# Optimization experiments

Hardware: AMD Instinct MI355X
Metric: run time of the kernel (lower is better)

## Reference

```python
import jax, jax.numpy as jnp
import numpy as np

EMB_DIM = 300
TEMPERATURE = 0.01
REWEIGHT = True
N = 8192
NUM_GROUPS = 100


def setup_inputs() -> dict:
    key = jax.random.key(0)
    ks = jax.random.split(key, 6)
    s = 1.0 / np.sqrt(EMB_DIM)
    x = jax.random.normal(ks[0], (N, EMB_DIM), dtype=jnp.float32)
    W1 = jax.random.normal(ks[1], (EMB_DIM, EMB_DIM), dtype=jnp.float32) * s
    b1 = jnp.zeros((EMB_DIM,), dtype=jnp.float32)
    W2 = jax.random.normal(ks[2], (EMB_DIM, EMB_DIM), dtype=jnp.float32) * s
    b2 = jnp.zeros((EMB_DIM,), dtype=jnp.float32)
    # labels in [1, 100]: all > 0 so the group_y>0 filter keeps every row
    labels = jax.random.randint(ks[3], (N,), 1, NUM_GROUPS + 1, dtype=jnp.int32)
    return {"x": x, "W1": W1, "b1": b1, "W2": W2, "b2": b2, "labels": labels}


def reference(x, W1, b1, W2, b2, labels):
    # projector: Linear -> ReLU -> Linear
    h = jax.nn.relu(x @ W1 + b1) @ W2 + b2
    # L2 normalize rows
    f = h / jnp.linalg.norm(h, axis=1, keepdims=True)
    # pairwise similarity / temperature, row-max subtracted (detached)
    logits = (f @ f.T) / TEMPERATURE                      # [N, N]
    logits = logits - jax.lax.stop_gradient(jnp.max(logits, axis=1, keepdims=True))

    lab = labels[:, None]
    mask = (lab == lab.T).astype(logits.dtype)            # same-group mask
    logits_mask = 1.0 - jnp.eye(mask.shape[0], dtype=logits.dtype)  # drop diagonal
    mask = mask * logits_mask

    # rows with at least one positive (torch filters these; we weight instead)
    pos_count = jnp.sum(mask, axis=1)                     # [N]
    valid = pos_count > 0

    if REWEIGHT:
        pos_m = logits_mask * mask
        neg_m = logits_mask * (1.0 - mask)
        pos_sum = jnp.sum(pos_m, axis=1, keepdims=True)
        neg_sum = jnp.sum(neg_m, axis=1, keepdims=True)
        log_pos = jnp.where(pos_sum > 0, jnp.log(jnp.maximum(pos_sum, 1.0)), 0.0)
        log_neg = jnp.where(neg_sum > 0, jnp.log(jnp.maximum(neg_sum, 1.0)), 0.0)
        logits = (logits - log_pos) * pos_m + (logits - log_neg) * neg_m

    exp_logits = jnp.exp(logits) * logits_mask
    log_prob = logits - jnp.log(jnp.sum(exp_logits, axis=1, keepdims=True))
    mean_log_prob_pos = jnp.sum(mask * log_prob, axis=1) / jnp.where(valid, pos_count, 1.0)
    validf = valid.astype(logits.dtype)
    loss = -TEMPERATURE * jnp.sum(mean_log_prob_pos * validf) / jnp.sum(validf)
    return loss
```

## Files before the change

kernel.cpp:

```cpp
#include <hip/hip_runtime.h>
#include <hip/hip_bf16.h>


#define N_ROWS 8192
#define D_PAD 320
#define NG 100
#define TEMP 0.01f
#define NSPLIT 32
#define JCHUNK (N_ROWS / NSPLIT)
#define LOG2E100 144.2695041f

typedef short short8v __attribute__((ext_vector_type(8)));
typedef float float4v __attribute__((ext_vector_type(4)));

__device__ __forceinline__ short f2bf(float f) {
  union { __hip_bfloat16 h; short s; } u;
  u.h = __float2bfloat16(f);
  return u.s;
}

__global__ __launch_bounds__(256) void setup_kernel(
    const float* __restrict__ W1, const float* __restrict__ W2,
    const int* __restrict__ labels,
    __hip_bfloat16* __restrict__ w1t, __hip_bfloat16* __restrict__ w2t,
    int* __restrict__ counts)
{
  __shared__ int hc[NG + 1];
  int b = blockIdx.x, tid = threadIdx.x;
  if (b < 800) {
    int isW2 = (b >= 400);
    int idx = (b - (isW2 ? 400 : 0)) * 256 + tid;
    const float* W = isW2 ? W2 : W1;
    __hip_bfloat16* dst = isW2 ? w2t : w1t;
    int n = idx / D_PAD, k = idx - n * D_PAD;
    float v = (n < 300 && k < 300) ? W[(size_t)k * 300 + n] : 0.0f;
    dst[idx] = __float2bfloat16(v);
  } else {
    if (tid <= NG) hc[tid] = 0;
    __syncthreads();
    int row = (b - 800) * 256 + tid;
    atomicAdd(&hc[labels[row]], 1);
    __syncthreads();
    if (tid <= NG && hc[tid] > 0) atomicAdd(&counts[tid], hc[tid]);
  }
}

__global__ __launch_bounds__(256, 2) void mlp_fused_kernel(
    const float* __restrict__ x, const __hip_bfloat16* __restrict__ w1t,
    const __hip_bfloat16* __restrict__ w2t, const float* __restrict__ b1,
    const float* __restrict__ b2, __hip_bfloat16* __restrict__ fb)
{
  __shared__ __align__(16) short Ws[64 * D_PAD];
  __shared__ __align__(16) short H1[64 * D_PAD];
  int tid = threadIdx.x;
  int lane = tid & 63, wave = tid >> 6;
  int g = lane >> 4, lc = lane & 15, sw = lc & 7;
  int i0 = blockIdx.x * 64;

  short8v afr[10];
  {
    const float* xp = x + (size_t)(i0 + wave * 16 + lc) * 300;
#pragma unroll
    for (int kk = 0; kk < 10; ++kk) {
      int k0 = kk * 32 + g * 8;
      short8v v;
      if (k0 + 8 <= 300) {
        float4 a = *(const float4*)(xp + k0);
        float4 c = *(const float4*)(xp + k0 + 4);
        v[0] = f2bf(a.x); v[1] = f2bf(a.y); v[2] = f2bf(a.z); v[3] = f2bf(a.w);
        v[4] = f2bf(c.x); v[5] = f2bf(c.y); v[6] = f2bf(c.z); v[7] = f2bf(c.w);
      } else if (k0 < 300) {
        float4 a = *(const float4*)(xp + k0);
        v[0] = f2bf(a.x); v[1] = f2bf(a.y); v[2] = f2bf(a.z); v[3] = f2bf(a.w);
        v[4] = 0; v[5] = 0; v[6] = 0; v[7] = 0;
      } else {
        v = short8v{0, 0, 0, 0, 0, 0, 0, 0};
      }
      afr[kk] = v;
    }
  }

  for (int c = 0; c < 5; ++c) {
    __syncthreads();
    {
      const int4* src = (const int4*)w1t;
      int4* dst = (int4*)Ws;
#pragma unroll
      for (int t = 0; t < 10; ++t) {
        int e = tid + t * 256;
        int r = e / 40, q = e - r * 40;
        dst[r * 40 + (q ^ (r & 7))] = src[(size_t)(c * 64 + r) * 40 + q];
      }
    }
    __syncthreads();
    for (int js = 0; js < 4; ++js) {
      float4v acc = {0.f, 0.f, 0.f, 0.f};
      const short* rowp = Ws + (js * 16 + lc) * D_PAD;
#pragma unroll
      for (int kk = 0; kk < 10; ++kk) {
        short8v bf = *(const short8v*)(rowp + (((g + 4 * kk) ^ sw) << 3));
        acc = __builtin_amdgcn_mfma_f32_16x16x32_bf16(afr[kk], bf, acc, 0, 0, 0);
      }
      int n = c * 64 + js * 16 + lc;
      float bv = (n < 300) ? b1[n] : 0.0f;
#pragma unroll
      for (int r = 0; r < 4; ++r) {
        int row = wave * 16 + g * 4 + r;
        int q = n >> 3;
        H1[row * D_PAD + ((q ^ (row & 7)) << 3) + (n & 7)] =
            f2bf(fmaxf(acc[r] + bv, 0.0f));
      }
    }
  }
  __syncthreads();

  short8v hfr[10];
  {
    const short* rp = H1 + (wave * 16 + lc) * D_PAD;
#pragma unroll
    for (int kk = 0; kk < 10; ++kk)
      hfr[kk] = *(const short8v*)(rp + (((g + 4 * kk) ^ sw) << 3));
  }

  float4v h2a[5][4];
  for (int c = 0; c < 5; ++c) {
    __syncthreads();
    {
      const int4* src = (const int4*)w2t;
      int4* dst = (int4*)Ws;
#pragma unroll
      for (int t = 0; t < 10; ++t) {
        int e = tid + t * 256;
        int r = e / 40, q = e - r * 40;
        dst[r * 40 + (q ^ (r & 7))] = src[(size_t)(c * 64 + r) * 40 + q];
      }
    }
    __syncthreads();
#pragma unroll
    for (int js = 0; js < 4; ++js) {
      float4v acc = {0.f, 0.f, 0.f, 0.f};
      const short* rowp = Ws + (js * 16 + lc) * D_PAD;
#pragma unroll
      for (int kk = 0; kk < 10; ++kk) {
        short8v bf = *(const short8v*)(rowp + (((g + 4 * kk) ^ sw) << 3));
        acc = __builtin_amdgcn_mfma_f32_16x16x32_bf16(hfr[kk], bf, acc, 0, 0, 0);
      }
      int n = c * 64 + js * 16 + lc;
      float bv = (n < 300) ? b2[n] : 0.0f;
#pragma unroll
      for (int r = 0; r < 4; ++r) acc[r] += bv;
      h2a[c][js] = acc;
    }
  }

  float ssq[4] = {0.f, 0.f, 0.f, 0.f};
#pragma unroll
  for (int c = 0; c < 5; ++c)
#pragma unroll
    for (int js = 0; js < 4; ++js)
#pragma unroll
      for (int r = 0; r < 4; ++r) ssq[r] = fmaf(h2a[c][js][r], h2a[c][js][r], ssq[r]);
  for (int m = 1; m < 16; m <<= 1)
#pragma unroll
    for (int r = 0; r < 4; ++r) ssq[r] += __shfl_xor(ssq[r], m, 64);
  float inv[4];
#pragma unroll
  for (int r = 0; r < 4; ++r) inv[r] = rsqrtf(ssq[r]);
#pragma unroll
  for (int c = 0; c < 5; ++c)
#pragma unroll
    for (int js = 0; js < 4; ++js) {
      int n = c * 64 + js * 16 + lc;
#pragma unroll
      for (int r = 0; r < 4; ++r) {
        int row = i0 + wave * 16 + g * 4 + r;
        fb[(size_t)row * D_PAD + n] = __float2bfloat16(h2a[c][js][r] * inv[r]);
      }
    }
}

__global__ __launch_bounds__(256) void group_kernel(
    const __hip_bfloat16* __restrict__ Fb, const int* __restrict__ labels,
    float* __restrict__ sPar, float* __restrict__ sAar)
{
  __shared__ __align__(16) short Bs[64 * D_PAD];
  __shared__ int memb[256];
  __shared__ int cnt;
  const short* Fs = (const short*)Fb;
  int tid = threadIdx.x;
  int lane = tid & 63, wave = tid >> 6;
  int g = lane >> 4, lc = lane & 15, sw = lc & 7;
  int grp = blockIdx.x + 1;
  if (tid == 0) cnt = 0;
  __syncthreads();
  for (int i = tid; i < N_ROWS; i += 256)
    if (labels[i] == grp) { int p = atomicAdd(&cnt, 1); if (p < 256) memb[p] = i; }
  __syncthreads();
  int c = cnt > 256 ? 256 : cnt;
  int nt = (c + 63) >> 6;
  for (int it = 0; it < nt; ++it) {
    short8v afr[10];
    {
      int islot = it * 64 + wave * 16 + lc;
      int arow = memb[islot < c ? islot : 0];
      const short* ap = Fs + (size_t)arow * D_PAD + g * 8;
#pragma unroll
      for (int kk = 0; kk < 10; ++kk) afr[kk] = *(const short8v*)(ap + kk * 32);
    }
    int iglobr[4]; bool ivalid[4];
    for (int r = 0; r < 4; ++r) {
      int islot = it * 64 + wave * 16 + g * 4 + r;
      ivalid[r] = islot < c;
      iglobr[r] = memb[islot < c ? islot : 0];
    }
    float sp[4] = {}, sa[4] = {};
    for (int jt = 0; jt < nt; ++jt) {
      __syncthreads();
      {
        const int4* src = (const int4*)Fs;
        int4* dst = (int4*)Bs;
#pragma unroll
        for (int t = 0; t < 10; ++t) {
          int e = tid + t * 256;
          int r = e / 40, q = e - r * 40;
          int jslot = jt * 64 + r;
          int grow = memb[jslot < c ? jslot : 0];
          dst[r * 40 + (q ^ (r & 7))] = src[(size_t)grow * 40 + q];
        }
      }
      __syncthreads();
      for (int js = 0; js < 4; ++js) {
        float4v acc = {0.f, 0.f, 0.f, 0.f};
        const short* rowp = Bs + (js * 16 + lc) * D_PAD;
#pragma unroll
        for (int kk = 0; kk < 10; ++kk) {
          short8v bf = *(const short8v*)(rowp + (((g + 4 * kk) ^ sw) << 3));
          acc = __builtin_amdgcn_mfma_f32_16x16x32_bf16(afr[kk], bf, acc, 0, 0, 0);
        }
        int jslot = jt * 64 + js * 16 + lc;
        bool jv = jslot < c;
        int jglob = memb[jslot < c ? jslot : 0];
#pragma unroll
        for (int r = 0; r < 4; ++r) {
          float a = acc[r];
          float e = exp2f(fmaf(a, LOG2E100, -LOG2E100));
          bool ok = jv && ivalid[r] && (jglob != iglobr[r]);
          sp[r] += ok ? e : 0.f;
          sa[r] += ok ? a : 0.f;
        }
      }
    }
    for (int m = 1; m < 16; m <<= 1)
      for (int r = 0; r < 4; ++r) {
        sp[r] += __shfl_xor(sp[r], m, 64);
        sa[r] += __shfl_xor(sa[r], m, 64);
      }
    if (lc == 0)
      for (int r = 0; r < 4; ++r)
        if (ivalid[r]) { sPar[iglobr[r]] = sp[r]; sAar[iglobr[r]] = sa[r]; }
  }
}

__global__ __launch_bounds__(256, 2) void pairwise_kernel(
    const __hip_bfloat16* __restrict__ Fb, float* __restrict__ partE)
{
  __shared__ __align__(16) short Bs[64 * D_PAD];
  const short* Fs = (const short*)Fb;
  int tid = threadIdx.x;
  int lane = tid & 63, wave = tid >> 6;
  int g = lane >> 4, lc = lane & 15, sw = lc & 7;
  int i0 = blockIdx.x * 128;
  int split = blockIdx.y;
  int jstart = split * JCHUNK;

  short8v afr[2][10];
  for (int s = 0; s < 2; ++s) {
    const short* ap = Fs + (size_t)(i0 + s * 64 + wave * 16 + lc) * D_PAD + g * 8;
#pragma unroll
    for (int kk = 0; kk < 10; ++kk) afr[s][kk] = *(const short8v*)(ap + kk * 32);
  }
  float sE[2][4] = {};

  for (int jt = 0; jt < JCHUNK / 64; ++jt) {
    int jb = jstart + jt * 64;
    __syncthreads();
    {
      const int4* src = (const int4*)Fs;
      int4* dst = (int4*)Bs;
#pragma unroll
      for (int t = 0; t < 10; ++t) {
        int e = tid + t * 256;
        int r = e / 40, q = e - r * 40;
        dst[r * 40 + (q ^ (r & 7))] = src[(size_t)(jb + r) * 40 + q];
      }
    }
    __syncthreads();
    for (int js = 0; js < 4; ++js) {
      float4v acc0 = {0.f, 0.f, 0.f, 0.f}, acc1 = {0.f, 0.f, 0.f, 0.f};
      const short* rowp = Bs + (js * 16 + lc) * D_PAD;
#pragma unroll
      for (int kk = 0; kk < 10; ++kk) {
        short8v bf = *(const short8v*)(rowp + (((g + 4 * kk) ^ sw) << 3));
        acc0 = __builtin_amdgcn_mfma_f32_16x16x32_bf16(afr[0][kk], bf, acc0, 0, 0, 0);
        acc1 = __builtin_amdgcn_mfma_f32_16x16x32_bf16(afr[1][kk], bf, acc1, 0, 0, 0);
      }
#pragma unroll
      for (int s = 0; s < 2; ++s) {
        float4v acc = s ? acc1 : acc0;
        bool dtile = (jb == i0 + s * 64) && (js == wave);
#pragma unroll
        for (int r = 0; r < 4; ++r) {
          float e = exp2f(fmaf(acc[r], LOG2E100, -LOG2E100));
          if (dtile && lc == g * 4 + r) e = 0.0f;
          sE[s][r] += e;
        }
      }
    }
  }
  for (int m = 1; m < 16; m <<= 1)
    for (int s = 0; s < 2; ++s)
      for (int r = 0; r < 4; ++r) sE[s][r] += __shfl_xor(sE[s][r], m, 64);
  if (lc == 0)
    for (int s = 0; s < 2; ++s)
      for (int r = 0; r < 4; ++r)
        partE[split * N_ROWS + i0 + s * 64 + wave * 16 + g * 4 + r] = sE[s][r];
}

__global__ __launch_bounds__(256) void final_a_kernel(
    const float* __restrict__ partE, const float* __restrict__ sPar,
    const float* __restrict__ sAar, const int* __restrict__ counts,
    const int* __restrict__ labels, float* __restrict__ blk)
{
  int tid = threadIdx.x;
  int i = blockIdx.x * 256 + tid;
  float sE = 0.f;
  for (int s = 0; s < NSPLIT; ++s) sE += partE[s * N_ROWS + i];
  float M = 0.f, V = 0.f;
  int pc = counts[labels[i]] - 1;
  if (pc > 0) {
    float P = sPar[i], A = sAar[i];
    float Q = sE - P;
    float pcf = (float)pc, ncf = (float)(N_ROWS - 1 - pc);
    float Z = P / pcf + Q / ncf;
    M = 100.0f * A / pcf - 100.0f - logf(pcf) - logf(Z);
    V = 1.f;
  }
  __shared__ float rm[256], rv[256];
  rm[tid] = M; rv[tid] = V;
  __syncthreads();
  for (int s2 = 128; s2 > 0; s2 >>= 1) {
    if (tid < s2) { rm[tid] += rm[tid + s2]; rv[tid] += rv[tid + s2]; }
    __syncthreads();
  }
  if (tid == 0) { blk[blockIdx.x] = rm[0]; blk[32 + blockIdx.x] = rv[0]; }
}

__global__ void final_b_kernel(const float* __restrict__ blk, float* __restrict__ out)
{
  int lane = threadIdx.x;
  float m = (lane < 32) ? blk[lane] : 0.f;
  float v = (lane < 32) ? blk[32 + lane] : 0.f;
  for (int s = 1; s < 32; s <<= 1) { m += __shfl_xor(m, s, 64); v += __shfl_xor(v, s, 64); }
  if (lane == 0) out[0] = (v > 0.f) ? (-TEMP * m / v) : 0.f;
}

extern "C" void kernel_launch(void* const* d_in, const int* in_sizes, int n_in,
                              void* d_out, int out_size, void* d_ws, size_t ws_size,
                              hipStream_t stream)
{
  const float* x  = (const float*)d_in[0];
  const float* W1 = (const float*)d_in[1];
  const float* b1 = (const float*)d_in[2];
  const float* W2 = (const float*)d_in[3];
  const float* b2 = (const float*)d_in[4];
  const int* labels = (const int*)d_in[5];

  char* ws = (char*)d_ws;
  __hip_bfloat16* fb  = (__hip_bfloat16*)(ws);
  __hip_bfloat16* w1t = (__hip_bfloat16*)(ws + 5242880);
  __hip_bfloat16* w2t = (__hip_bfloat16*)(ws + 5447680);
  int*         counts = (int*)(ws + 5652480);
  float*        partE = (float*)(ws + 5652992);
  float*        sPar  = (float*)(ws + 6701568);
  float*        sAar  = (float*)(ws + 6734336);
  float*        blk   = (float*)(ws + 6767104);

  hipMemsetAsync(counts, 0, (NG + 1) * sizeof(int), stream);
  setup_kernel<<<832, 256, 0, stream>>>(W1, W2, labels, w1t, w2t, counts);
  mlp_fused_kernel<<<N_ROWS / 64, 256, 0, stream>>>(x, w1t, w2t, b1, b2, fb);
  group_kernel<<<NG, 256, 0, stream>>>(fb, labels, sPar, sAar);
  pairwise_kernel<<<dim3(N_ROWS / 128, NSPLIT), 256, 0, stream>>>(fb, partE);
  final_a_kernel<<<32, 256, 0, stream>>>(partE, sPar, sAar, counts, labels, blk);
  final_b_kernel<<<1, 64, 0, stream>>>(blk, (float*)d_out);
}
```

Measured before the change: 174.8 us.

## Exploit Gram symmetry, fuse group and pairwise kernels, merge final reductions

The pairwise exp-sum kernel now computes only upper-triangular 128x128 tiles and adds each tile's column sums into the mirrored rows with atomics, roughly halving the MFMA and exp work. The group kernel runs inside the same launch as extra blocks so both overlap. The weight transpose uses an LDS tile for coalesced access, the MLP kernel uses 32-row blocks with 128 threads for more blocks, and the two final reduction kernels become one. Atomics on row sums add contention, and early-returning blocks waste part of the grid.

Measured after the change: 233.5 us. +33.6%, slower.

```diff
diff --git a/kernel.cpp b/kernel.cpp
--- a/kernel.cpp
+++ b/kernel.cpp
@@ -6,8 +6,6 @@
 #define D_PAD 320
 #define NG 100
 #define TEMP 0.01f
-#define NSPLIT 32
-#define JCHUNK (N_ROWS / NSPLIT)
 #define LOG2E100 144.2695041f
 
 typedef short short8v __attribute__((ext_vector_type(8)));
@@ -25,37 +23,50 @@
     __hip_bfloat16* __restrict__ w1t, __hip_bfloat16* __restrict__ w2t,
     int* __restrict__ counts)
 {
+  __shared__ float T[64][65];
   __shared__ int hc[NG + 1];
   int b = blockIdx.x, tid = threadIdx.x;
-  if (b < 800) {
-    int isW2 = (b >= 400);
-    int idx = (b - (isW2 ? 400 : 0)) * 256 + tid;
+  if (b < 50) {
+    int isW2 = b >= 25;
+    int t5 = isW2 ? b - 25 : b;
+    int k0 = (t5 / 5) * 64, n0 = (t5 % 5) * 64;
     const float* W = isW2 ? W2 : W1;
     __hip_bfloat16* dst = isW2 ? w2t : w1t;
-    int n = idx / D_PAD, k = idx - n * D_PAD;
-    float v = (n < 300 && k < 300) ? W[(size_t)k * 300 + n] : 0.0f;
-    dst[idx] = __float2bfloat16(v);
+#pragma unroll
+    for (int t = 0; t < 16; ++t) {
+      int e = tid + t * 256;
+      int r = e >> 6, c = e & 63;
+      T[r][c] = (k0 + r < 300 && n0 + c < 300)
+                  ? W[(size_t)(k0 + r) * 300 + (n0 + c)] : 0.0f;
+    }
+    __syncthreads();
+#pragma unroll
+    for (int t = 0; t < 16; ++t) {
+      int e = tid + t * 256;
+      int nn = e >> 6, kk = e & 63;
+      dst[(size_t)(n0 + nn) * D_PAD + (k0 + kk)] = __float2bfloat16(T[kk][nn]);
+    }
   } else {
     if (tid <= NG) hc[tid] = 0;
     __syncthreads();
-    int row = (b - 800) * 256 + tid;
+    int row = (b - 50) * 256 + tid;
     atomicAdd(&hc[labels[row]], 1);
     __syncthreads();
     if (tid <= NG && hc[tid] > 0) atomicAdd(&counts[tid], hc[tid]);
   }
 }
 
-__global__ __launch_bounds__(256, 2) void mlp_fused_kernel(
+__global__ __launch_bounds__(128, 2) void mlp_fused_kernel(
     const float* __restrict__ x, const __hip_bfloat16* __restrict__ w1t,
     const __hip_bfloat16* __restrict__ w2t, const float* __restrict__ b1,
     const float* __restrict__ b2, __hip_bfloat16* __restrict__ fb)
 {
   __shared__ __align__(16) short Ws[64 * D_PAD];
-  __shared__ __align__(16) short H1[64 * D_PAD];
+  __shared__ __align__(16) short H1[32 * D_PAD];
   int tid = threadIdx.x;
   int lane = tid & 63, wave = tid >> 6;
   int g = lane >> 4, lc = lane & 15, sw = lc & 7;
-  int i0 = blockIdx.x * 64;
+  int i0 = blockIdx.x * 32;
 
   short8v afr[10];
   {
@@ -86,8 +97,8 @@
       const int4* src = (const int4*)w1t;
       int4* dst = (int4*)Ws;
 #pragma unroll
-      for (int t = 0; t < 10; ++t) {
-        int e = tid + t * 256;
+      for (int t = 0; t < 20; ++t) {
+        int e = tid + t * 128;
         int r = e / 40, q = e - r * 40;
         dst[r * 40 + (q ^ (r & 7))] = src[(size_t)(c * 64 + r) * 40 + q];
       }
@@ -129,8 +140,8 @@
       const int4* src = (const int4*)w2t;
       int4* dst = (int4*)Ws;
 #pragma unroll
-      for (int t = 0; t < 10; ++t) {
-        int e = tid + t * 256;
+      for (int t = 0; t < 20; ++t) {
+        int e = tid + t * 128;
         int r = e / 40, q = e - r * 40;
         dst[r * 40 + (q ^ (r & 7))] = src[(size_t)(c * 64 + r) * 40 + q];
       }
@@ -179,42 +190,37 @@
     }
 }
 
-__global__ __launch_bounds__(256) void group_kernel(
+__global__ __launch_bounds__(256, 2) void pg_kernel(
     const __hip_bfloat16* __restrict__ Fb, const int* __restrict__ labels,
-    float* __restrict__ sPar, float* __restrict__ sAar)
+    float* __restrict__ sEar, float* __restrict__ sPar, float* __restrict__ sAar)
 {
   __shared__ __align__(16) short Bs[64 * D_PAD];
+  __shared__ float colAcc[128];
   __shared__ int memb[256];
   __shared__ int cnt;
   const short* Fs = (const short*)Fb;
   int tid = threadIdx.x;
   int lane = tid & 63, wave = tid >> 6;
   int g = lane >> 4, lc = lane & 15, sw = lc & 7;
-  int grp = blockIdx.x + 1;
-  if (tid == 0) cnt = 0;
-  __syncthreads();
-  for (int i = tid; i < N_ROWS; i += 256)
-    if (labels[i] == grp) { int p = atomicAdd(&cnt, 1); if (p < 256) memb[p] = i; }
-  __syncthreads();
-  int c = cnt > 256 ? 256 : cnt;
-  int nt = (c + 63) >> 6;
-  for (int it = 0; it < nt; ++it) {
-    short8v afr[10];
-    {
-      int islot = it * 64 + wave * 16 + lc;
-      int arow = memb[islot < c ? islot : 0];
-      const short* ap = Fs + (size_t)arow * D_PAD + g * 8;
-#pragma unroll
-      for (int kk = 0; kk < 10; ++kk) afr[kk] = *(const short8v*)(ap + kk * 32);
-    }
-    int iglobr[4]; bool ivalid[4];
-    for (int r = 0; r < 4; ++r) {
-      int islot = it * 64 + wave * 16 + g * 4 + r;
-      ivalid[r] = islot < c;
-      iglobr[r] = memb[islot < c ? islot : 0];
-    }
-    float sp[4] = {}, sa[4] = {};
-    for (int jt = 0; jt < nt; ++jt) {
+  int b = blockIdx.x;
+
+  if (b < 4096) {
+    int bi = b >> 6, bj = b & 63;
+    if (bj < bi) return;
+    bool diag = (bi == bj);
+    int i0 = bi * 128, j0 = bj * 128;
+    if (tid < 128) colAcc[tid] = 0.f;
+
+    short8v afr[2][10];
+    for (int s = 0; s < 2; ++s) {
+      const short* ap = Fs + (size_t)(i0 + s * 64 + wave * 16 + lc) * D_PAD + g * 8;
+#pragma unroll
+      for (int kk = 0; kk < 10; ++kk) afr[s][kk] = *(const short8v*)(ap + kk * 32);
+    }
+    float sE[2][4] = {};
+
+    for (int jt = 0; jt < 2; ++jt) {
+      int jb = j0 + jt * 64;
       __syncthreads();
       {
         const int4* src = (const int4*)Fs;
@@ -223,145 +229,151 @@
         for (int t = 0; t < 10; ++t) {
           int e = tid + t * 256;
           int r = e / 40, q = e - r * 40;
-          int jslot = jt * 64 + r;
-          int grow = memb[jslot < c ? jslot : 0];
-          dst[r * 40 + (q ^ (r & 7))] = src[(size_t)grow * 40 + q];
+          dst[r * 40 + (q ^ (r & 7))] = src[(size_t)(jb + r) * 40 + q];
         }
       }
       __syncthreads();
       for (int js = 0; js < 4; ++js) {
-        float4v acc = {0.f, 0.f, 0.f, 0.f};
+        float4v acc0 = {0.f, 0.f, 0.f, 0.f}, acc1 = {0.f, 0.f, 0.f, 0.f};
         const short* rowp = Bs + (js * 16 + lc) * D_PAD;
 #pragma unroll
         for (int kk = 0; kk < 10; ++kk) {
           short8v bf = *(const short8v*)(rowp + (((g + 4 * kk) ^ sw) << 3));
-          acc = __builtin_amdgcn_mfma_f32_16x16x32_bf16(afr[kk], bf, acc, 0, 0, 0);
-        }
-        int jslot = jt * 64 + js * 16 + lc;
-        bool jv = jslot < c;
-        int jglob = memb[jslot < c ? jslot : 0];
-#pragma unroll
+          acc0 = __builtin_amdgcn_mfma_f32_16x16x32_bf16(afr[0][kk], bf, acc0, 0, 0, 0);
+          acc1 = __builtin_amdgcn_mfma_f32_16x16x32_bf16(afr[1][kk], bf, acc1, 0, 0, 0);
+        }
+#pragma unroll
+        for (int s = 0; s < 2; ++s) {
+          float4v acc = s ? acc1 : acc0;
+          bool dt = diag && (jt == s) && (js == wave);
+          float cs = 0.f;
+#pragma unroll
+          for (int r = 0; r < 4; ++r) {
+            float e = exp2f(fmaf(acc[r], LOG2E100, -LOG2E100));
+            if (dt && lc == g * 4 + r) e = 0.0f;
+            sE[s][r] += e;
+            cs += e;
+          }
+          if (!diag) {
+            cs += __shfl_xor(cs, 16, 64);
+            cs += __shfl_xor(cs, 32, 64);
+            if (g == 0) atomicAdd(&colAcc[jt * 64 + js * 16 + lc], cs);
+          }
+        }
+      }
+    }
+    for (int m = 1; m < 16; m <<= 1)
+#pragma unroll
+      for (int s = 0; s < 2; ++s)
+#pragma unroll
+        for (int r = 0; r < 4; ++r) sE[s][r] += __shfl_xor(sE[s][r], m, 64);
+    if (lc == 0)
+      for (int s = 0; s < 2; ++s)
+        for (int r = 0; r < 4; ++r)
+          atomicAdd(&sEar[i0 + s * 64 + wave * 16 + g * 4 + r], sE[s][r]);
+    if (!diag) {
+      __syncthreads();
+      if (tid < 128) atomicAdd(&sEar[j0 + tid], colAcc[tid]);
+    }
+  } else {
+    int grp = b - 4096 + 1;
+    if (tid == 0) cnt = 0;
+    __syncthreads();
+    for (int i = tid; i < N_ROWS; i += 256)
+      if (labels[i] == grp) { int p = atomicAdd(&cnt, 1); if (p < 256) memb[p] = i; }
+    __syncthreads();
+    int c = cnt > 256 ? 256 : cnt;
+    int nt = (c + 63) >> 6;
+    for (int it = 0; it < nt; ++it) {
+      short8v afr[10];
+      {
+        int islot = it * 64 + wave * 16 + lc;
+        int arow = memb[islot < c ? islot : 0];
+        const short* ap = Fs + (size_t)arow * D_PAD + g * 8;
+#pragma unroll
+        for (int kk = 0; kk < 10; ++kk) afr[kk] = *(const short8v*)(ap + kk * 32);
+      }
+      int iglobr[4]; bool ivalid[4];
+      for (int r = 0; r < 4; ++r) {
+        int islot = it * 64 + wave * 16 + g * 4 + r;
+        ivalid[r] = islot < c;
+        iglobr[r] = memb[islot < c ? islot : 0];
+      }
+      float sp[4] = {}, sa[4] = {};
+      for (int jt = 0; jt < nt; ++jt) {
+        __syncthreads();
+        {
+          const int4* src = (const int4*)Fs;
+          int4* dst = (int4*)Bs;
+#pragma unroll
+          for (int t = 0; t < 10; ++t) {
+            int e = tid + t * 256;
+            int r = e / 40, q = e - r * 40;
+            int jslot = jt * 64 + r;
+            int grow = memb[jslot < c ? jslot : 0];
+            dst[r * 40 + (q ^ (r & 7))] = src[(size_t)grow * 40 + q];
+          }
+        }
+        __syncthreads();
+        for (int js = 0; js < 4; ++js) {
+          float4v acc = {0.f, 0.f, 0.f, 0.f};
+          const short* rowp = Bs + (js * 16 + lc) * D_PAD;
+#pragma unroll
+          for (int kk = 0; kk < 10; ++kk) {
+            short8v bf = *(const short8v*)(rowp + (((g + 4 * kk) ^ sw) << 3));
+            acc = __builtin_amdgcn_mfma_f32_16x16x32_bf16(afr[kk], bf, acc, 0, 0, 0);
+          }
+          int jslot = jt * 64 + js * 16 + lc;
+          bool jv = jslot < c;
+          int jglob = memb[jslot < c ? jslot : 0];
+#pragma unroll
+          for (int r = 0; r < 4; ++r) {
+            float a = acc[r];
+            float e = exp2f(fmaf(a, LOG2E100, -LOG2E100));
+            bool ok = jv && ivalid[r] && (jglob != iglobr[r]);
+            sp[r] += ok ? e : 0.f;
+            sa[r] += ok ? a : 0.f;
+          }
+        }
+      }
+      for (int m = 1; m < 16; m <<= 1)
         for (int r = 0; r < 4; ++r) {
-          float a = acc[r];
-          float e = exp2f(fmaf(a, LOG2E100, -LOG2E100));
-          bool ok = jv && ivalid[r] && (jglob != iglobr[r]);
-          sp[r] += ok ? e : 0.f;
-          sa[r] += ok ? a : 0.f;
-        }
-      }
-    }
-    for (int m = 1; m < 16; m <<= 1)
-      for (int r = 0; r < 4; ++r) {
-        sp[r] += __shfl_xor(sp[r], m, 64);
-        sa[r] += __shfl_xor(sa[r], m, 64);
-      }
-    if (lc == 0)
-      for (int r = 0; r < 4; ++r)
-        if (ivalid[r]) { sPar[iglobr[r]] = sp[r]; sAar[iglobr[r]] = sa[r]; }
-  }
-}
-
-__global__ __launch_bounds__(256, 2) void pairwise_kernel(
-    const __hip_bfloat16* __restrict__ Fb, float* __restrict__ partE)
-{
-  __shared__ __align__(16) short Bs[64 * D_PAD];
-  const short* Fs = (const short*)Fb;
-  int tid = threadIdx.x;
-  int lane = tid & 63, wave = tid >> 6;
-  int g = lane >> 4, lc = lane & 15, sw = lc & 7;
-  int i0 = blockIdx.x * 128;
-  int split = blockIdx.y;
-  int jstart = split * JCHUNK;
-
-  short8v afr[2][10];
-  for (int s = 0; s < 2; ++s) {
-    const short* ap = Fs + (size_t)(i0 + s * 64 + wave * 16 + lc) * D_PAD + g * 8;
-#pragma unroll
-    for (int kk = 0; kk < 10; ++kk) afr[s][kk] = *(const short8v*)(ap + kk * 32);
-  }
-  float sE[2][4] = {};
-
-  for (int jt = 0; jt < JCHUNK / 64; ++jt) {
-    int jb = jstart + jt * 64;
-    __syncthreads();
-    {
-      const int4* src = (const int4*)Fs;
-      int4* dst = (int4*)Bs;
-#pragma unroll
-      for (int t = 0; t < 10; ++t) {
-        int e = tid + t * 256;
-        int r = e / 40, q = e - r * 40;
-        dst[r * 40 + (q ^ (r & 7))] = src[(size_t)(jb + r) * 40 + q];
-      }
-    }
-    __syncthreads();
-    for (int js = 0; js < 4; ++js) {
-      float4v acc0 = {0.f, 0.f, 0.f, 0.f}, acc1 = {0.f, 0.f, 0.f, 0.f};
-      const short* rowp = Bs + (js * 16 + lc) * D_PAD;
-#pragma unroll
-      for (int kk = 0; kk < 10; ++kk) {
-        short8v bf = *(const short8v*)(rowp + (((g + 4 * kk) ^ sw) << 3));
-        acc0 = __builtin_amdgcn_mfma_f32_16x16x32_bf16(afr[0][kk], bf, acc0, 0, 0, 0);
-        acc1 = __builtin_amdgcn_mfma_f32_16x16x32_bf16(afr[1][kk], bf, acc1, 0, 0, 0);
-      }
-#pragma unroll
-      for (int s = 0; s < 2; ++s) {
-        float4v acc = s ? acc1 : acc0;
-        bool dtile = (jb == i0 + s * 64) && (js == wave);
-#pragma unroll
-        for (int r = 0; r < 4; ++r) {
-          float e = exp2f(fmaf(acc[r], LOG2E100, -LOG2E100));
-          if (dtile && lc == g * 4 + r) e = 0.0f;
-          sE[s][r] += e;
-        }
-      }
-    }
-  }
-  for (int m = 1; m < 16; m <<= 1)
-    for (int s = 0; s < 2; ++s)
-      for (int r = 0; r < 4; ++r) sE[s][r] += __shfl_xor(sE[s][r], m, 64);
-  if (lc == 0)
-    for (int s = 0; s < 2; ++s)
-      for (int r = 0; r < 4; ++r)
-        partE[split * N_ROWS + i0 + s * 64 + wave * 16 + g * 4 + r] = sE[s][r];
-}
-
-__global__ __launch_bounds__(256) void final_a_kernel(
-    const float* __restrict__ partE, const float* __restrict__ sPar,
+          sp[r] += __shfl_xor(sp[r], m, 64);
+          sa[r] += __shfl_xor(sa[r], m, 64);
+        }
+      if (lc == 0)
+        for (int r = 0; r < 4; ++r)
+          if (ivalid[r]) { sPar[iglobr[r]] = sp[r]; sAar[iglobr[r]] = sa[r]; }
+    }
+  }
+}
+
+__global__ __launch_bounds__(1024) void final_kernel(
+    const float* __restrict__ sEar, const float* __restrict__ sPar,
     const float* __restrict__ sAar, const int* __restrict__ counts,
-    const int* __restrict__ labels, float* __restrict__ blk)
+    const int* __restrict__ labels, float* __restrict__ out)
 {
   int tid = threadIdx.x;
-  int i = blockIdx.x * 256 + tid;
-  float sE = 0.f;
-  for (int s = 0; s < NSPLIT; ++s) sE += partE[s * N_ROWS + i];
-  float M = 0.f, V = 0.f;
-  int pc = counts[labels[i]] - 1;
-  if (pc > 0) {
-    float P = sPar[i], A = sAar[i];
-    float Q = sE - P;
-    float pcf = (float)pc, ncf = (float)(N_ROWS - 1 - pc);
-    float Z = P / pcf + Q / ncf;
-    M = 100.0f * A / pcf - 100.0f - logf(pcf) - logf(Z);
-    V = 1.f;
-  }
-  __shared__ float rm[256], rv[256];
-  rm[tid] = M; rv[tid] = V;
+  float sumM = 0.f, sumV = 0.f;
+  for (int i = tid; i < N_ROWS; i += 1024) {
+    int pc = counts[labels[i]] - 1;
+    if (pc > 0) {
+      float P = sPar[i], A = sAar[i];
+      float Q = sEar[i] - P;
+      float pcf = (float)pc, ncf = (float)(N_ROWS - 1 - pc);
+      float Z = P / pcf + Q / ncf;
+      sumM += 100.0f * A / pcf - 100.0f - logf(pcf) - logf(Z);
+      sumV += 1.f;
+    }
+  }
+  __shared__ float rm[1024], rv[1024];
+  rm[tid] = sumM; rv[tid] = sumV;
   __syncthreads();
-  for (int s2 = 128; s2 > 0; s2 >>= 1) {
-    if (tid < s2) { rm[tid] += rm[tid + s2]; rv[tid] += rv[tid + s2]; }
-    __syncthreads();
-  }
-  if (tid == 0) { blk[blockIdx.x] = rm[0]; blk[32 + blockIdx.x] = rv[0]; }
-}
-
-__global__ void final_b_kernel(const float* __restrict__ blk, float* __restrict__ out)
-{
-  int lane = threadIdx.x;
-  float m = (lane < 32) ? blk[lane] : 0.f;
-  float v = (lane < 32) ? blk[32 + lane] : 0.f;
-  for (int s = 1; s < 32; s <<= 1) { m += __shfl_xor(m, s, 64); v += __shfl_xor(v, s, 64); }
-  if (lane == 0) out[0] = (v > 0.f) ? (-TEMP * m / v) : 0.f;
+  for (int s = 512; s > 0; s >>= 1) {
+    if (tid < s) { rm[tid] += rm[tid + s]; rv[tid] += rv[tid + s]; }
+    __syncthreads();
+  }
+  if (tid == 0) out[0] = (rv[0] > 0.f) ? (-TEMP * rm[0] / rv[0]) : 0.f;
 }
 
 extern "C" void kernel_launch(void* const* d_in, const int* in_sizes, int n_in,
@@ -380,16 +392,14 @@
   __hip_bfloat16* w1t = (__hip_bfloat16*)(ws + 5242880);
   __hip_bfloat16* w2t = (__hip_bfloat16*)(ws + 5447680);
   int*         counts = (int*)(ws + 5652480);
-  float*        partE = (float*)(ws + 5652992);
-  float*        sPar  = (float*)(ws + 6701568);
-  float*        sAar  = (float*)(ws + 6734336);
-  float*        blk   = (float*)(ws + 6767104);
-
-  hipMemsetAsync(counts, 0, (NG + 1) * sizeof(int), stream);
-  setup_kernel<<<832, 256, 0, stream>>>(W1, W2, labels, w1t, w2t, counts);
-  mlp_fused_kernel<<<N_ROWS / 64, 256, 0, stream>>>(x, w1t, w2t, b1, b2, fb);
-  group_kernel<<<NG, 256, 0, stream>>>(fb, labels, sPar, sAar);
-  pairwise_kernel<<<dim3(N_ROWS / 128, NSPLIT), 256, 0, stream>>>(fb, partE);
-  final_a_kernel<<<32, 256, 0, stream>>>(partE, sPar, sAar, counts, labels, blk);
-  final_b_kernel<<<1, 64, 0, stream>>>(blk, (float*)d_out);
-}
+  float*        sEar  = (float*)(ws + 5652992);
+  float*        sPar  = (float*)(ws + 5685760);
+  float*        sAar  = (float*)(ws + 5718528);
+  
+  hipMemsetAsync(counts, 0, 512, stream);
+  hipMemsetAsync(sEar, 0, N_ROWS * sizeof(float), stream);
+  setup_kernel<<<82, 256, 0, stream>>>(W1, W2, labels, w1t, w2t, counts);
+  mlp_fused_kernel<<<256, 128, 0, stream>>>(x, w1t, w2t, b1, b2, fb);
+  pg_kernel<<<4096 + NG, 256, 0, stream>>>(fb, labels, sEar, sPar, sAar);
+  final_kernel<<<1, 1024, 0, stream>>>(sEar, sPar, sAar, counts, labels, (float*)d_out);
+}
```
